# Kernel optimization log

Hardware: AMD Instinct MI355X
Metric: run time of the kernel (lower is better)

The kernel has to match this reference:

```python
import jax, jax.numpy as jnp
import numpy as np

NUM_CLASSES = 81
TOP_K = 200
CONF_THRESH = 0.01
NMS_THRESH = 0.45
VAR0, VAR1 = 0.1, 0.2  # SSD Config['variance']


def decode(loc, priors):
    # loc: [..., P, 4], priors: [P, 4] (cx, cy, w, h)
    cxcy = priors[:, :2] + loc[..., :2] * VAR0 * priors[:, 2:]
    wh = priors[:, 2:] * jnp.exp(loc[..., 2:] * VAR1)
    x1y1 = cxcy - wh * 0.5
    x2y2 = x1y1 + wh
    return jnp.concatenate([x1y1, x2y2], axis=-1)  # [..., P, 4] xyxy


def nms_class(boxes, scores):
    # boxes: [P, 4], scores: [P] -> [TOP_K, 5] rows of (score, x1, y1, x2, y2)
    K = TOP_K
    masked = jnp.where(scores > CONF_THRESH, scores, -jnp.inf)
    top_scores, idx = jax.lax.top_k(masked, K)          # descending
    cand = boxes[idx]                                   # [K, 4]
    valid = jnp.isfinite(top_scores)
    x1, y1, x2, y2 = cand[:, 0], cand[:, 1], cand[:, 2], cand[:, 3]
    area = (x2 - x1) * (y2 - y1)
    iw = jnp.maximum(jnp.minimum(x2[:, None], x2[None, :]) - jnp.maximum(x1[:, None], x1[None, :]), 0.0)
    ih = jnp.maximum(jnp.minimum(y2[:, None], y2[None, :]) - jnp.maximum(y1[:, None], y1[None, :]), 0.0)
    inter = iw * ih
    union = area[:, None] + area[None, :] - inter
    iou = jnp.where(union > 0, inter / jnp.where(union > 0, union, 1.0), 0.0)  # [K, K]
    ar = jnp.arange(K)

    def step(suppressed, i):
        kept = valid[i] & ~suppressed[i]
        suppressed = suppressed | (kept & (iou[i] > NMS_THRESH) & (ar > i))
        return suppressed, kept

    _, keep = jax.lax.scan(step, jnp.zeros(K, dtype=bool), ar)  # [K] bool
    rows = jnp.concatenate([jnp.where(valid, top_scores, 0.0)[:, None], cand], axis=1)  # [K, 5]
    # compact kept rows to the front (score-descending order), zeros after
    tgt = jnp.where(keep, jnp.cumsum(keep) - 1, K)
    out = jnp.zeros((K + 1, 5), rows.dtype).at[tgt].set(rows)[:K]
    return out


def detect(loc_data, conf_data, prior_data):
    boxes = decode(loc_data, prior_data)                 # [B, P, 4]
    conf = jnp.transpose(conf_data, (0, 2, 1))           # [B, C, P]
    per_image = jax.vmap(nms_class, in_axes=(None, 0))   # over classes
    out = jax.vmap(per_image, in_axes=(0, 0))(boxes, conf)  # [B, C, K, 5]
    out = out.at[:, 0].set(0.0)  # background class skipped (cl starts at 1)
    return out


def setup_inputs() -> dict:
    key = jax.random.key(0)
    k1, k2, k3 = jax.random.split(key, 3)
    B, P, C = 32, 24564, NUM_CLASSES
    loc_data = jax.random.normal(k1, (B, P, 4), dtype=jnp.float32)
    conf_data = jax.random.uniform(k2, (B, P, C), dtype=jnp.float32)
    prior_data = jax.random.uniform(k3, (P, 4), dtype=jnp.float32)
    return {"loc_data": loc_data, "conf_data": conf_data, "prior_data": prior_data}


def reference(loc_data, conf_data, prior_data):
    return detect(loc_data, conf_data, prior_data)
```

## Files before the change

kernel.cpp:

```cpp
#include <hip/hip_runtime.h>
#include <hip/hip_bf16.h>
#include <math.h>

constexpr int B_ = 32;
constexpr int P_ = 24564;
constexpr int C_ = 81;
constexpr int K_ = 200;

constexpr int NCH = 64;
constexpr int CPR = 384;
constexpr int SCAP = 1024;
constexpr int CAP  = 512;
constexpr int NSORT = 512;
constexpr float T_SEL = 0.9869f;

__global__ __launch_bounds__(256) void k_filter(const float* __restrict__ conf,
                                                unsigned long long* __restrict__ cand,
                                                unsigned* __restrict__ cnt,
                                                unsigned* __restrict__ bflag) {
    __shared__ unsigned long long skey[SCAP];
    __shared__ unsigned short scls[SCAP];
    __shared__ unsigned scnt[C_], sbase[C_], scnt2[C_];
    __shared__ unsigned sn;
    const int bid = blockIdx.x;
    const int b = bid / NCH, ch = bid % NCH;
    const int tid = threadIdx.x;

    for (int i = tid; i < C_; i += 256) { scnt[i] = 0; scnt2[i] = 0; }
    if (tid == 0) sn = 0;
    __syncthreads();

    const int p0 = ch * CPR;
    const int rows = min(CPR, P_ - p0);
    const float* slab = conf + ((size_t)b * P_ + (size_t)p0) * C_;
    const int n4 = rows * C_ / 4;
    for (int g = tid; g < n4; g += 256) {
        float4 v = ((const float4*)slab)[g];
        int e = g * 4;
        int c = e % C_;
        int pl = e / C_;
        float s[4] = {v.x, v.y, v.z, v.w};
#pragma unroll
        for (int j = 0; j < 4; ++j) {
            int cj = c + j, pj = pl;
            if (cj >= C_) { cj -= C_; pj += 1; }
            float sv = s[j];
            if (sv > T_SEL && cj != 0) {
                unsigned pos = atomicAdd(&sn, 1u);
                if (pos < (unsigned)SCAP) {
                    unsigned pg = (unsigned)(p0 + pj);
                    skey[pos] = ((unsigned long long)__float_as_uint(sv) << 32) | (~pg);
                    scls[pos] = (unsigned short)cj;
                    atomicAdd(&scnt[cj], 1u);
                } else {
                    bflag[b] = 1u;
                }
            }
        }
    }
    __syncthreads();
    if (tid < C_) sbase[tid] = scnt[tid] ? atomicAdd(&cnt[b * C_ + tid], scnt[tid]) : 0u;
    __syncthreads();
    const int m = (int)min(sn, (unsigned)SCAP);
    for (int i = tid; i < m; i += 256) {
        int c = scls[i];
        unsigned pos = sbase[c] + atomicAdd(&scnt2[c], 1u);
        if (pos < (unsigned)CAP)
            cand[((size_t)(b * C_ + c)) * CAP + pos] = skey[i];
    }
}

__global__ __launch_bounds__(256) void k_nms(const unsigned long long* __restrict__ cand,
                                             const unsigned* __restrict__ cnt,
                                             const unsigned* __restrict__ bflag,
                                             const float* __restrict__ conf,
                                             const float* __restrict__ loc,
                                             const float* __restrict__ prior,
                                             float* __restrict__ out) {
#pragma clang fp contract(off)
    __shared__ __align__(16) unsigned long long masks[K_][4];
    __shared__ __align__(16) float outrow[1024];
    __shared__ unsigned long long top[256];
    __shared__ float sc[K_], bx1[K_], by1[K_], bx2[K_], by2[K_], bar[K_];
    __shared__ unsigned char vflag[K_];
    __shared__ unsigned long long keepw[4];
    __shared__ unsigned kpre[4];
    __shared__ unsigned long long sh_prefix;
    __shared__ unsigned sh_rank, sh_cnt2, sh_cut, sh_fat;

    unsigned long long* buf = (unsigned long long*)outrow;
    unsigned* rs_hist = (unsigned*)&masks[0][0];
    unsigned* rs_sf   = rs_hist + 256;

    const int bid = blockIdx.x;
    const int b = bid / C_, c = bid % C_;
    const int tid = threadIdx.x;
    float* obase = out + ((size_t)(b * C_ + c)) * (K_ * 5);

    if (c == 0) {
        float4 z = make_float4(0.f, 0.f, 0.f, 0.f);
        for (int i = tid; i < K_ * 5 / 4; i += 256) ((float4*)obase)[i] = z;
        return;
    }

    const int task = b * C_ + c;
    const unsigned long long* crow = cand + (size_t)task * CAP;
    const unsigned cn = cnt[task];
    const bool fb = (bflag[b] != 0u) || (cn < (unsigned)K_) || (cn > (unsigned)CAP);

    int n;
    if (!fb) {
        n = (int)cn;
    } else {
        for (int i = tid; i < NSORT; i += 256) buf[i] = 0ull;
        const float* col = conf + (size_t)b * P_ * C_ + c;
        unsigned lc = 0;
        for (int p = tid; p < P_; p += 256)
            if (col[(size_t)p * C_] > 0.01f) lc++;
        rs_sf[tid] = lc;
        __syncthreads();
        for (int off = 128; off > 0; off >>= 1) {
            if (tid < off) rs_sf[tid] += rs_sf[tid + off];
            __syncthreads();
        }
        const unsigned total = rs_sf[0];
        unsigned long long t200v = 1ull;
        if (total > (unsigned)K_) {
            if (tid == 0) { sh_prefix = 0ull; sh_rank = (unsigned)K_; }
            __syncthreads();
            for (int d = 7; d >= 0; --d) {
                rs_hist[tid] = 0;
                __syncthreads();
                const unsigned long long pref = sh_prefix;
                const unsigned rank = sh_rank;
                for (int p = tid; p < P_; p += 256) {
                    float sv = col[(size_t)p * C_];
                    if (sv > 0.01f) {
                        unsigned long long key =
                            ((unsigned long long)__float_as_uint(sv) << 32) | (~(unsigned)p);
                        bool match = (d == 7) || (((key ^ pref) >> ((d + 1) * 8)) == 0ull);
                        if (match) atomicAdd(&rs_hist[(unsigned)((key >> (d * 8)) & 255ull)], 1u);
                    }
                }
                __syncthreads();
                rs_sf[tid] = rs_hist[tid];
                __syncthreads();
                for (int off = 1; off < 256; off <<= 1) {
                    unsigned v2 = (tid + off < 256) ? rs_sf[tid + off] : 0u;
                    __syncthreads();
                    rs_sf[tid] += v2;
                    __syncthreads();
                }
                if (rs_sf[tid] >= rank && (tid == 255 || rs_sf[tid + 1] < rank)) {
                    sh_prefix = pref | ((unsigned long long)tid << (d * 8));
                    sh_rank = rank - ((tid == 255) ? 0u : rs_sf[tid + 1]);
                }
                __syncthreads();
            }
            t200v = sh_prefix;
        }
        if (tid == 0) sh_cnt2 = 0;
        __syncthreads();
        for (int p = tid; p < P_; p += 256) {
            float sv = col[(size_t)p * C_];
            if (sv > 0.01f) {
                unsigned long long key =
                    ((unsigned long long)__float_as_uint(sv) << 32) | (~(unsigned)p);
                if (key >= t200v) {
                    unsigned pos = atomicAdd(&sh_cnt2, 1u);
                    if (pos < (unsigned)CAP) buf[pos] = key;
                }
            }
        }
        __syncthreads();
        n = (int)min(sh_cnt2, (unsigned)CAP);
    }

    bool fat = false;
    if (n <= 256) {
        top[tid] = (tid < n) ? (fb ? buf[tid] : crow[tid]) : 0ull;
        __syncthreads();
    } else {
        if (tid == 0) { sh_fat = 0u; sh_cnt2 = 0u; }
        rs_hist[tid] = 0u;
        __syncthreads();
        for (int i = tid; i < n; i += 256)
            atomicAdd(&rs_hist[(unsigned)((crow[i] >> 43) & 255ull)], 1u);
        __syncthreads();
        rs_sf[tid] = rs_hist[tid];
        __syncthreads();
        for (int off = 1; off < 256; off <<= 1) {
            unsigned v2 = (tid + off < 256) ? rs_sf[tid + off] : 0u;
            __syncthreads();
            rs_sf[tid] += v2;
            __syncthreads();
        }
        if (rs_sf[tid] >= (unsigned)K_ && (tid == 255 || rs_sf[tid + 1] < (unsigned)K_)) {
            sh_cut = (unsigned)tid;
            sh_fat = (rs_sf[tid] > 256u) ? 1u : 0u;
        }
        __syncthreads();
        fat = (sh_fat != 0u);
        if (!fat) {
            const unsigned cut = sh_cut;
            top[tid] = 0ull;
            __syncthreads();
            for (int i = tid; i < n; i += 256) {
                unsigned long long key = crow[i];
                if ((unsigned)((key >> 43) & 255ull) >= cut)
                    top[atomicAdd(&sh_cnt2, 1u)] = key;
            }
            __syncthreads();
        } else {
            for (int i = tid; i < NSORT; i += 256)
                buf[i] = (i < n) ? crow[i] : 0ull;
            __syncthreads();
        }
    }

    if (!fat) {
        bool after_cross = false;
        for (int k = 2; k <= 256; k <<= 1) {
            for (int j = k >> 1; j > 0; j >>= 1) {
                bool cross = (j >= 128);
                if (cross || after_cross) __syncthreads();
                else asm volatile("" ::: "memory");
                if (tid < 128) {
                    int e = ((tid & ~(j - 1)) << 1) | (tid & (j - 1));
                    int pp = e | j;
                    bool up = ((e & k) == 0);
                    unsigned long long a = top[e], bb = top[pp];
                    unsigned long long lo = a < bb ? a : bb;
                    unsigned long long hi = a < bb ? bb : a;
                    top[e]  = up ? lo : hi;
                    top[pp] = up ? hi : lo;
                }
                asm volatile("" ::: "memory");
                after_cross = cross;
            }
        }
        __syncthreads();
    } else {
        for (int k = 2; k <= NSORT; k <<= 1) {
            for (int j = k >> 1; j > 0; j >>= 1) {
                __syncthreads();
                int e = ((tid & ~(j - 1)) << 1) | (tid & (j - 1));
                int pp = e | j;
                bool up = ((e & k) == 0);
                unsigned long long a = buf[e], bb = buf[pp];
                unsigned long long lo = a < bb ? a : bb;
                unsigned long long hi = a < bb ? bb : a;
                buf[e]  = up ? lo : hi;
                buf[pp] = up ? hi : lo;
            }
        }
        __syncthreads();
    }

    const int nsel = min(n, K_);
    const unsigned long long* srt = fat ? buf : top;
    const int srtN = fat ? NSORT : 256;

    if (tid < K_) {
        const int r = tid;
        bool v = (r < nsel);
        float score = 0.f, x1 = 0.f, y1 = 0.f, x2 = 0.f, y2 = 0.f, ar = 0.f;
        if (v) {
            unsigned long long key = srt[srtN - 1 - r];
            unsigned ub = (unsigned)(key >> 32);
            unsigned p = ~((unsigned)key);
            score = __uint_as_float(ub);
            v = ((ub & 0x7F800000u) != 0x7F800000u);
            const float4 l4 = ((const float4*)loc)[(size_t)b * P_ + p];
            const float4 p4 = ((const float4*)prior)[p];
            float cx = p4.x + (l4.x * 0.1f) * p4.z;
            float cy = p4.y + (l4.y * 0.1f) * p4.w;
            float w  = p4.z * expf(l4.z * 0.2f);
            float h  = p4.w * expf(l4.w * 0.2f);
            x1 = cx - w * 0.5f;
            y1 = cy - h * 0.5f;
            x2 = x1 + w;
            y2 = y1 + h;
            ar = (x2 - x1) * (y2 - y1);
        }
        sc[r] = score; bx1[r] = x1; by1[r] = y1; bx2[r] = x2; by2[r] = y2; bar[r] = ar;
        vflag[r] = v ? (unsigned char)1 : (unsigned char)0;
    }
    __syncthreads();

    for (int i = tid; i < 1024; i += 256) outrow[i] = 0.0f;

    const int nv = nsel;
    const int wid = tid >> 6, lane = tid & 63;

    float jx1[4], jy1[4], jx2[4], jy2[4], jar[4];
#pragma unroll
    for (int w = 0; w < 4; ++w) {
        int j = w * 64 + lane;
        bool in = (j < K_);
        jx1[w] = in ? bx1[j] : 0.f;
        jy1[w] = in ? by1[j] : 0.f;
        jx2[w] = in ? bx2[j] : 0.f;
        jy2[w] = in ? by2[j] : 0.f;
        jar[w] = in ? bar[j] : 0.f;
    }

    for (int idx = tid; idx < K_ * 4; idx += 256) {
        int i = idx >> 2, w = idx & 3;
        if (w < (i >> 6)) masks[i][w] = 0ull;
    }
    for (int i = wid; i < nv; i += 4) {
        float r_x1 = bx1[i], r_y1 = by1[i], r_x2 = bx2[i], r_y2 = by2[i], r_ar = bar[i];
        const int w0 = i >> 6;
#pragma unroll
        for (int w = 0; w < 4; ++w) {
            if (w >= w0) {
                int j = w * 64 + lane;
                bool pred = false;
                if (j < nv && j > i) {
                    float xx1 = fmaxf(r_x1, jx1[w]);
                    float yy1 = fmaxf(r_y1, jy1[w]);
                    float xx2 = fminf(r_x2, jx2[w]);
                    float yy2 = fminf(r_y2, jy2[w]);
                    float iw = fmaxf(xx2 - xx1, 0.0f);
                    float ih = fmaxf(yy2 - yy1, 0.0f);
                    float inter = iw * ih;
                    float uni = (r_ar + jar[w]) - inter;
                    pred = (uni > 0.0f) && (inter / uni > 0.45f);
                }
                unsigned long long m = __ballot(pred);
                if (lane == 0) masks[i][w] = m;
            }
        }
    }
    __syncthreads();

    if (tid < 64) {
        const int l = tid;
        unsigned long long V0 = __ballot((l       < nv) && vflag[l]);
        unsigned long long V1 = __ballot((64 + l  < nv) && vflag[64 + l]);
        unsigned long long V2 = __ballot((128 + l < nv) && vflag[128 + l]);
        unsigned long long V3 = __ballot((192 + l < nv) && vflag[192 + l]);
        auto rownz = [&](int r) -> bool {
            if (r >= nv) return false;
            return (masks[r][0] | masks[r][1] | masks[r][2] | masks[r][3]) != 0ull;
        };
        unsigned long long R0 = __ballot(rownz(l))       & V0;
        unsigned long long R1 = __ballot(rownz(64 + l))  & V1;
        unsigned long long R2 = __ballot(rownz(128 + l)) & V2;
        unsigned long long R3 = __ballot(rownz(192 + l)) & V3;

        unsigned long long S0 = 0, S1 = 0, S2 = 0, S3 = 0;
        while (true) {
            unsigned long long t;
            int i = -1;
            if ((t = R0 & ~S0) != 0ull)      i = (int)__builtin_ctzll(t);
            else if ((t = R1 & ~S1) != 0ull) i = 64 + (int)__builtin_ctzll(t);
            else if ((t = R2 & ~S2) != 0ull) i = 128 + (int)__builtin_ctzll(t);
            else if ((t = R3 & ~S3) != 0ull) i = 192 + (int)__builtin_ctzll(t);
            if (i < 0) break;
            const unsigned long long bit = 1ull << (i & 63);
            const int slot = i >> 6;
            if (slot == 0) R0 ^= bit; else if (slot == 1) R1 ^= bit;
            else if (slot == 2) R2 ^= bit; else R3 ^= bit;
            ulonglong2 m01 = *(const ulonglong2*)&masks[i][0];
            ulonglong2 m23 = *(const ulonglong2*)&masks[i][2];
            S0 |= m01.x; S1 |= m01.y; S2 |= m23.x; S3 |= m23.y;
        }
        if (l == 0) {
            unsigned long long K0 = V0 & ~S0, K1 = V1 & ~S1, K2 = V2 & ~S2, K3 = V3 & ~S3;
            keepw[0] = K0; keepw[1] = K1; keepw[2] = K2; keepw[3] = K3;
            kpre[0] = 0;
            kpre[1] = (unsigned)__popcll(K0);
            kpre[2] = kpre[1] + (unsigned)__popcll(K1);
            kpre[3] = kpre[2] + (unsigned)__popcll(K2);
        }
    }
    __syncthreads();

    if (tid < nv) {
        int w = tid >> 6, bit = tid & 63;
        if ((keepw[w] >> bit) & 1ull) {
            unsigned slot = kpre[w] + (unsigned)__popcll(keepw[w] & ((1ull << bit) - 1ull));
            outrow[slot * 5 + 0] = sc[tid];
            outrow[slot * 5 + 1] = bx1[tid];
            outrow[slot * 5 + 2] = by1[tid];
            outrow[slot * 5 + 3] = bx2[tid];
            outrow[slot * 5 + 4] = by2[tid];
        }
    }
    __syncthreads();

    for (int i = tid; i < K_ * 5 / 4; i += 256)
        ((float4*)obase)[i] = ((const float4*)outrow)[i];
}

extern "C" void kernel_launch(void* const* d_in, const int* in_sizes, int n_in,
                              void* d_out, int out_size, void* d_ws, size_t ws_size,
                              hipStream_t stream) {
    const float* loc   = (const float*)d_in[0];
    const float* conf  = (const float*)d_in[1];
    const float* prior = (const float*)d_in[2];
    float* out = (float*)d_out;

    char* ws = (char*)d_ws;
    const size_t candBytes = (size_t)B_ * C_ * CAP * sizeof(unsigned long long);
    unsigned long long* cand = (unsigned long long*)ws;
    unsigned* cnt   = (unsigned*)(ws + candBytes);
    unsigned* bflag = cnt + (size_t)B_ * C_;

    hipMemsetAsync(cnt, 0, (size_t)(B_ * C_ + B_) * sizeof(unsigned), stream);

    k_filter<<<B_ * NCH, 256, 0, stream>>>(conf, cand, cnt, bflag);
    k_nms   <<<B_ * C_,  256, 0, stream>>>(cand, cnt, bflag, conf, loc, prior, out);
}
```

Measured before the change: 159.6 us.

## Replace bitonic sort of candidates with rank-by-counting selection

Instead of a histogram cut followed by a 256- or 512-element bitonic sort with many barriers, each thread takes up to two candidate keys and computes each key's rank by counting how many buffered keys are larger. It then scatters the key directly into the top array in descending order. This removes the many __syncthreads of the sorting network and the histogram pass, at the cost of O(n) shared-memory reads per thread (up to 512 keys read as 128-bit vectors). Keys are unique because the index is packed into the low bits, so ranks do not collide.

```diff
diff --git a/kernel.cpp b/kernel.cpp
--- a/kernel.cpp
+++ b/kernel.cpp
@@ -11,7 +11,6 @@
 constexpr int CPR = 384;
 constexpr int SCAP = 1024;
 constexpr int CAP  = 512;
-constexpr int NSORT = 512;
 constexpr float T_SEL = 0.9869f;
 
 __global__ __launch_bounds__(256) void k_filter(const float* __restrict__ conf,
@@ -86,7 +85,7 @@
     __shared__ unsigned long long keepw[4];
     __shared__ unsigned kpre[4];
     __shared__ unsigned long long sh_prefix;
-    __shared__ unsigned sh_rank, sh_cnt2, sh_cut, sh_fat;
+    __shared__ unsigned sh_rank, sh_cnt2;
 
     unsigned long long* buf = (unsigned long long*)outrow;
     unsigned* rs_hist = (unsigned*)&masks[0][0];
@@ -111,8 +110,13 @@
     int n;
     if (!fb) {
         n = (int)cn;
+        for (int i = tid; i < CAP; i += 256)
+            buf[i] = (i < n) ? crow[i] : 0ull;
+        top[tid] = 0ull;
+        __syncthreads();
     } else {
-        for (int i = tid; i < NSORT; i += 256) buf[i] = 0ull;
+        for (int i = tid; i < CAP; i += 256) buf[i] = 0ull;
+        top[tid] = 0ull;
         const float* col = conf + (size_t)b * P_ * C_ + c;
         unsigned lc = 0;
         for (int p = tid; p < P_; p += 256)
@@ -176,97 +180,30 @@
         n = (int)min(sh_cnt2, (unsigned)CAP);
     }
 
-    bool fat = false;
-    if (n <= 256) {
-        top[tid] = (tid < n) ? (fb ? buf[tid] : crow[tid]) : 0ull;
-        __syncthreads();
-    } else {
-        if (tid == 0) { sh_fat = 0u; sh_cnt2 = 0u; }
-        rs_hist[tid] = 0u;
-        __syncthreads();
-        for (int i = tid; i < n; i += 256)
-            atomicAdd(&rs_hist[(unsigned)((crow[i] >> 43) & 255ull)], 1u);
-        __syncthreads();
-        rs_sf[tid] = rs_hist[tid];
-        __syncthreads();
-        for (int off = 1; off < 256; off <<= 1) {
-            unsigned v2 = (tid + off < 256) ? rs_sf[tid + off] : 0u;
-            __syncthreads();
-            rs_sf[tid] += v2;
-            __syncthreads();
-        }
-        if (rs_sf[tid] >= (unsigned)K_ && (tid == 255 || rs_sf[tid + 1] < (unsigned)K_)) {
-            sh_cut = (unsigned)tid;
-            sh_fat = (rs_sf[tid] > 256u) ? 1u : 0u;
-        }
-        __syncthreads();
-        fat = (sh_fat != 0u);
-        if (!fat) {
-            const unsigned cut = sh_cut;
-            top[tid] = 0ull;
-            __syncthreads();
-            for (int i = tid; i < n; i += 256) {
-                unsigned long long key = crow[i];
-                if ((unsigned)((key >> 43) & 255ull) >= cut)
-                    top[atomicAdd(&sh_cnt2, 1u)] = key;
-            }
-            __syncthreads();
-        } else {
-            for (int i = tid; i < NSORT; i += 256)
-                buf[i] = (i < n) ? crow[i] : 0ull;
-            __syncthreads();
-        }
-    }
-
-    if (!fat) {
-        bool after_cross = false;
-        for (int k = 2; k <= 256; k <<= 1) {
-            for (int j = k >> 1; j > 0; j >>= 1) {
-                bool cross = (j >= 128);
-                if (cross || after_cross) __syncthreads();
-                else asm volatile("" ::: "memory");
-                if (tid < 128) {
-                    int e = ((tid & ~(j - 1)) << 1) | (tid & (j - 1));
-                    int pp = e | j;
-                    bool up = ((e & k) == 0);
-                    unsigned long long a = top[e], bb = top[pp];
-                    unsigned long long lo = a < bb ? a : bb;
-                    unsigned long long hi = a < bb ? bb : a;
-                    top[e]  = up ? lo : hi;
-                    top[pp] = up ? hi : lo;
-                }
-                asm volatile("" ::: "memory");
-                after_cross = cross;
-            }
-        }
-        __syncthreads();
-    } else {
-        for (int k = 2; k <= NSORT; k <<= 1) {
-            for (int j = k >> 1; j > 0; j >>= 1) {
-                __syncthreads();
-                int e = ((tid & ~(j - 1)) << 1) | (tid & (j - 1));
-                int pp = e | j;
-                bool up = ((e & k) == 0);
-                unsigned long long a = buf[e], bb = buf[pp];
-                unsigned long long lo = a < bb ? a : bb;
-                unsigned long long hi = a < bb ? bb : a;
-                buf[e]  = up ? lo : hi;
-                buf[pp] = up ? hi : lo;
-            }
-        }
-        __syncthreads();
-    }
+    {
+        const unsigned long long k1 = buf[tid];
+        const unsigned long long k2 = buf[tid + 256];
+        int r1 = 0, r2 = 0;
+        const int nn = (n + 3) & ~3;
+        for (int i = 0; i < nn; i += 4) {
+            ulonglong2 a = *(const ulonglong2*)&buf[i];
+            ulonglong2 bb = *(const ulonglong2*)&buf[i + 2];
+            r1 += (a.x > k1) + (a.y > k1) + (bb.x > k1) + (bb.y > k1);
+            r2 += (a.x > k2) + (a.y > k2) + (bb.x > k2) + (bb.y > k2);
+        }
+        if (k1 != 0ull && r1 < 256) top[r1] = k1;
+        if (k2 != 0ull && r2 < 256) top[r2] = k2;
+    }
+    __syncthreads();
 
     const int nsel = min(n, K_);
-    const unsigned long long* srt = fat ? buf : top;
-    const int srtN = fat ? NSORT : 256;
 
     if (tid < K_) {
         const int r = tid;
         bool v = (r < nsel);
         float score = 0.f, x1 = 0.f, y1 = 0.f, x2 = 0.f, y2 = 0.f, ar = 0.f;
         if (v) {
-            unsigned long long key = srt[srtN - 1 - r];
+            unsigned long long key = top[r];
             unsigned ub = (unsigned)(key >> 32);
             unsigned p = ~((unsigned)key);
             score = __uint_as_float(ub);
```

New measurement: 167.1 us. +4.7%, slower.
